# Kernel optimization log

Measured on AMD Instinct MI355X. Metric: run time of the kernel, lower is better.

## Reference

```python
import jax, jax.numpy as jnp
import numpy as np
import math

# AAMsoftmax constants (m=0.2, s=30), matching the torch implementation
M = 0.2
S = 30.0
COS_M = math.cos(M)
SIN_M = math.sin(M)
TH = math.cos(math.pi - M)
MM = math.sin(math.pi - M) * M

B, IN, P, C = 4096, 1024, 256, 5994


def _l2norm(v):
    # F.normalize: v / max(||v||, eps)
    n = jnp.sqrt(jnp.sum(v * v, axis=-1, keepdims=True))
    return v / jnp.maximum(n, 1e-12)


def setup_inputs() -> dict:
    key = jax.random.key(0)
    k0, k1, k2, k3 = jax.random.split(key, 4)
    return {
        "x": jax.random.normal(k0, (B, IN), jnp.float32),
        "label": jax.random.randint(k1, (B,), 0, C, dtype=jnp.int32),
        "W_fc": jax.random.normal(k2, (P, IN), jnp.float32) * (1.0 / np.sqrt(IN)),
        "b_fc": jnp.zeros((P,), jnp.float32),
        "W_aam": jax.random.normal(k3, (C, P), jnp.float32) * 0.05,
    }


def reference(x, label, W_fc, b_fc, W_aam):
    # fc layer: [B, IN] -> [B, P]
    e = x @ W_fc.T + b_fc
    # cosine similarity against class prototypes: [B, C]
    cosine = _l2norm(e) @ _l2norm(W_aam).T
    sine = jnp.sqrt(jnp.clip(1.0 - cosine * cosine, 0.0, 1.0))
    phi = cosine * COS_M - sine * SIN_M
    # easy-margin-off fallback: use cosine - mm where angle too large
    phi = jnp.where((cosine - TH) > 0, phi, cosine - MM)
    one_hot = jax.nn.one_hot(label, C, dtype=cosine.dtype)
    logits = (one_hot * phi + (1.0 - one_hot) * cosine) * S
    # cross-entropy (mean over batch)
    logp = jax.nn.log_softmax(logits, axis=-1)
    nll = -jnp.take_along_axis(logp, label[:, None].astype(jnp.int32), axis=1)[:, 0]
    return jnp.mean(nll)
```

## Files before the change

### kernel.cpp

```cpp
#include <hip/hip_runtime.h>
#include <math.h>

typedef __attribute__((ext_vector_type(8))) short bf16x8;
typedef __attribute__((ext_vector_type(4))) float f32x4;

#define AAM_COS_M 0.9800665778412416f
#define AAM_SIN_M 0.19866933079506122f
#define AAM_TH   (-0.9800665778412416f)
#define AAM_MM    0.03973386615901225f
#define C_CLS 5994

__device__ inline ushort f2bf(float f) {
    unsigned x = __float_as_uint(f);
    return (ushort)((x + 0x7fffu + ((x >> 16) & 1u)) >> 16);
}
__device__ inline float bflo(unsigned u) { return __uint_as_float(u << 16); }
__device__ inline float bfhi(unsigned u) { return __uint_as_float(u & 0xffff0000u); }

__device__ __forceinline__ void gload16(const void* g, void* lds) {
    __builtin_amdgcn_global_load_lds(
        (const __attribute__((address_space(1))) unsigned int*)g,
        (__attribute__((address_space(3))) unsigned int*)lds, 16, 0, 0);
}

__global__ __launch_bounds__(256) void conv_bf16(const float* __restrict__ x,
                                                 const float* __restrict__ Wfc,
                                                 ushort* __restrict__ xb,
                                                 ushort* __restrict__ wb) {
    int b = blockIdx.x;
    const float* s; ushort* d; int i;
    if (b < 4096) { s = x; d = xb; i = b * 256 + threadIdx.x; }
    else          { s = Wfc; d = wb; i = (b - 4096) * 256 + threadIdx.x; }
    float4 v = ((const float4*)s)[i];
    ushort4 o;
    o.x = f2bf(v.x); o.y = f2bf(v.y); o.z = f2bf(v.z); o.w = f2bf(v.w);
    ((ushort4*)d)[i] = o;
}

__global__ __launch_bounds__(256) void fc_mfma(const ushort* __restrict__ A,
                                               const ushort* __restrict__ Bm,
                                               const float* __restrict__ bias,
                                               float* __restrict__ C) {
    __shared__ ushort As[64 * 32];
    __shared__ ushort Bs[64 * 32];
    const int tid = threadIdx.x, lane = tid & 63, w = tid >> 6;
    const int wr = w >> 1, wc = w & 1;
    const int lx = lane & 15, lg = lane >> 4;
    const int l4 = lane >> 2, c8 = (lane & 3) << 3;
    const int rb = blockIdx.x * 64, cb = blockIdx.y * 64;

    f32x4 zero = {0.f, 0.f, 0.f, 0.f};
    f32x4 acc[2][2];
#pragma unroll
    for (int i = 0; i < 2; ++i)
#pragma unroll
        for (int j = 0; j < 2; ++j) acc[i][j] = zero;

    for (int k0 = 0; k0 < 1024; k0 += 32) {
        gload16(&A[(size_t)(rb + w * 16 + l4) * 1024 + k0 + c8], &As[w * 512]);
        gload16(&Bm[(size_t)(cb + w * 16 + l4) * 1024 + k0 + c8], &Bs[w * 512]);
        __syncthreads();
        bf16x8 af[2], bv[2];
#pragma unroll
        for (int f = 0; f < 2; ++f) {
            af[f] = *(const bf16x8*)&As[(wr * 32 + f * 16 + lx) * 32 + lg * 8];
            bv[f] = *(const bf16x8*)&Bs[(wc * 32 + f * 16 + lx) * 32 + lg * 8];
        }
#pragma unroll
        for (int i = 0; i < 2; ++i)
#pragma unroll
            for (int j = 0; j < 2; ++j)
                acc[i][j] = __builtin_amdgcn_mfma_f32_16x16x32_bf16(af[i], bv[j], acc[i][j], 0, 0, 0);
        __syncthreads();
    }
#pragma unroll
    for (int j = 0; j < 2; ++j) {
        int col = cb + wc * 32 + j * 16 + lx;
        float bb = bias[col];
#pragma unroll
        for (int i = 0; i < 2; ++i) {
            int row0 = rb + wr * 32 + i * 16 + lg * 4;
#pragma unroll
            for (int r = 0; r < 4; ++r)
                C[(size_t)(row0 + r) * 256 + col] = acc[i][j][r] + bb;
        }
    }
}

__global__ __launch_bounds__(256) void rownorm_e(const float* __restrict__ E,
                                                 ushort* __restrict__ En) {
    const int wave = threadIdx.x >> 6, lane = threadIdx.x & 63;
    const int row = blockIdx.x * 4 + wave;
    float4 v = ((const float4*)&E[(size_t)row * 256])[lane];
    float ss = v.x * v.x + v.y * v.y + v.z * v.z + v.w * v.w;
#pragma unroll
    for (int m = 32; m >= 1; m >>= 1) ss += __shfl_xor(ss, m, 64);
    float sc = 1.f / fmaxf(sqrtf(ss), 1e-12f);
    ushort4 o;
    o.x = f2bf(v.x * sc); o.y = f2bf(v.y * sc); o.z = f2bf(v.z * sc); o.w = f2bf(v.w * sc);
    ((ushort4*)&En[(size_t)row * 256])[lane] = o;
}

__global__ __launch_bounds__(256) void rownorm_w(const float* __restrict__ W,
                                                 ushort* __restrict__ Wn) {
    const int wave = threadIdx.x >> 6, lane = threadIdx.x & 63;
    const int row = blockIdx.x * 4 + wave;
    if (row >= 6144) return;
    ushort4 o;
    if (row < C_CLS) {
        float4 v = ((const float4*)&W[(size_t)row * 256])[lane];
        float ss = v.x * v.x + v.y * v.y + v.z * v.z + v.w * v.w;
#pragma unroll
        for (int m = 32; m >= 1; m >>= 1) ss += __shfl_xor(ss, m, 64);
        float sc = 1.f / fmaxf(sqrtf(ss), 1e-12f);
        o.x = f2bf(v.x * sc); o.y = f2bf(v.y * sc); o.z = f2bf(v.z * sc); o.w = f2bf(v.w * sc);
    } else {
        o.x = 0; o.y = 0; o.z = 0; o.w = 0;
    }
    ((ushort4*)&Wn[(size_t)row * 256])[lane] = o;
}

__global__ __launch_bounds__(256) void aam_mfma(const ushort* __restrict__ A,
                                                const ushort* __restrict__ Bm,
                                                float* __restrict__ pm,
                                                float* __restrict__ ps) {
    __shared__ ushort As[128 * 32];
    __shared__ ushort Bs[128 * 32];
    const int tid = threadIdx.x, lane = tid & 63, w = tid >> 6;
    const int wr = w >> 1, wc = w & 1;
    const int lx = lane & 15, lg = lane >> 4;
    const int l4 = lane >> 2, c8 = (lane & 3) << 3;
    const int rb = blockIdx.x * 128;
    const int split = blockIdx.y;

    float mrun[16], srun[16];
#pragma unroll
    for (int idx = 0; idx < 16; ++idx) { mrun[idx] = -INFINITY; srun[idx] = 0.f; }

    f32x4 zero = {0.f, 0.f, 0.f, 0.f};
    for (int t = 0; t < 3; ++t) {
        const int cb = split * 384 + t * 128;
        f32x4 acc[4][4];
#pragma unroll
        for (int i = 0; i < 4; ++i)
#pragma unroll
            for (int j = 0; j < 4; ++j) acc[i][j] = zero;

        for (int k0 = 0; k0 < 256; k0 += 32) {
            gload16(&A[(size_t)(rb + w * 32 + l4) * 256 + k0 + c8], &As[w * 1024]);
            gload16(&A[(size_t)(rb + w * 32 + 16 + l4) * 256 + k0 + c8], &As[w * 1024 + 512]);
            gload16(&Bm[(size_t)(cb + w * 32 + l4) * 256 + k0 + c8], &Bs[w * 1024]);
            gload16(&Bm[(size_t)(cb + w * 32 + 16 + l4) * 256 + k0 + c8], &Bs[w * 1024 + 512]);
            __syncthreads();
            bf16x8 af[4], bv[4];
#pragma unroll
            for (int f = 0; f < 4; ++f) {
                af[f] = *(const bf16x8*)&As[(wr * 64 + f * 16 + lx) * 32 + lg * 8];
                bv[f] = *(const bf16x8*)&Bs[(wc * 64 + f * 16 + lx) * 32 + lg * 8];
            }
#pragma unroll
            for (int i = 0; i < 4; ++i)
#pragma unroll
                for (int j = 0; j < 4; ++j)
                    acc[i][j] = __builtin_amdgcn_mfma_f32_16x16x32_bf16(af[i], bv[j], acc[i][j], 0, 0, 0);
            __syncthreads();
        }

#pragma unroll
        for (int j = 0; j < 4; ++j) {
            int c = cb + wc * 64 + j * 16 + lx;
            if (c < C_CLS) {
#pragma unroll
                for (int i = 0; i < 4; ++i)
#pragma unroll
                    for (int r = 0; r < 4; ++r) {
                        float v = 30.f * acc[i][j][r];
                        int idx = i * 4 + r;
                        float mn = fmaxf(mrun[idx], v);
                        srun[idx] = srun[idx] * __expf(mrun[idx] - mn) + __expf(v - mn);
                        mrun[idx] = mn;
                    }
            }
        }
    }

#pragma unroll
    for (int idx = 0; idx < 16; ++idx) {
#pragma unroll
        for (int msk = 1; msk < 16; msk <<= 1) {
            float om = __shfl_xor(mrun[idx], msk, 64);
            float os = __shfl_xor(srun[idx], msk, 64);
            float mn = fmaxf(mrun[idx], om);
            float sa = (mrun[idx] > -1e37f) ? srun[idx] * __expf(mrun[idx] - mn) : 0.f;
            float sb = (om > -1e37f) ? os * __expf(om - mn) : 0.f;
            mrun[idx] = mn; srun[idx] = sa + sb;
        }
        if (lx == 0) {
            int row = rb + wr * 64 + (idx >> 2) * 16 + lg * 4 + (idx & 3);
            int part = split * 2 + wc;
            pm[part * 4096 + row] = mrun[idx];
            ps[part * 4096 + row] = srun[idx];
        }
    }
}

__global__ __launch_bounds__(256) void reduce_all(const float* __restrict__ pm,
                                                  const float* __restrict__ ps,
                                                  const ushort* __restrict__ En,
                                                  const ushort* __restrict__ Wn,
                                                  const int* __restrict__ lab,
                                                  float* __restrict__ partial) {
    __shared__ float red[4];
    const int wave = threadIdx.x >> 6, lane = threadIdx.x & 63;
    const int gw = blockIdx.x * 4 + wave;
    float acc = 0.f;
#pragma unroll
    for (int r = 0; r < 4; ++r) {
        const int row = gw * 4 + r;
        const int l = lab[row];
        uint2 a = ((const uint2*)&En[(size_t)row * 256])[lane];
        uint2 b = ((const uint2*)&Wn[(size_t)l * 256])[lane];
        float sum = bflo(a.x) * bflo(b.x) + bfhi(a.x) * bfhi(b.x)
                  + bflo(a.y) * bflo(b.y) + bfhi(a.y) * bfhi(b.y);
#pragma unroll
        for (int m = 32; m >= 1; m >>= 1) sum += __shfl_xor(sum, m, 64);
        float cv = sum;

        float m, s;
        if (lane < 32) { m = pm[lane * 4096 + row]; s = ps[lane * 4096 + row]; }
        else           { m = -INFINITY; s = 0.f; }
#pragma unroll
        for (int msk = 1; msk <= 32; msk <<= 1) {
            float om = __shfl_xor(m, msk, 64);
            float os = __shfl_xor(s, msk, 64);
            float mn = fmaxf(m, om);
            float sa = (m > -1e37f) ? s * __expf(m - mn) : 0.f;
            float sb = (om > -1e37f) ? os * __expf(om - mn) : 0.f;
            m = mn; s = sa + sb;
        }
        float sine = sqrtf(fmaxf(1.f - cv * cv, 0.f));
        float phi = cv * AAM_COS_M - sine * AAM_SIN_M;
        phi = ((cv - AAM_TH) > 0.f) ? phi : (cv - AAM_MM);
        float vplain = 30.f * cv, vlab = 30.f * phi;
        float denom = s - __expf(vplain - m) + __expf(vlab - m);
        acc += m + logf(denom) - vlab;
    }
    if (lane == 0) red[wave] = acc;
    __syncthreads();
    if (threadIdx.x == 0)
        partial[blockIdx.x] = red[0] + red[1] + red[2] + red[3];
}

__global__ __launch_bounds__(256) void final_reduce(const float* __restrict__ partial,
                                                    float* __restrict__ out) {
    __shared__ float red[4];
    const int wave = threadIdx.x >> 6, lane = threadIdx.x & 63;
    float v = partial[threadIdx.x];
#pragma unroll
    for (int m = 32; m >= 1; m >>= 1) v += __shfl_xor(v, m, 64);
    if (lane == 0) red[wave] = v;
    __syncthreads();
    if (threadIdx.x == 0)
        out[0] = (red[0] + red[1] + red[2] + red[3]) * (1.f / 4096.f);
}

extern "C" void kernel_launch(void* const* d_in, const int* in_sizes, int n_in,
                              void* d_out, int out_size, void* d_ws, size_t ws_size,
                              hipStream_t stream) {
    const float* x    = (const float*)d_in[0];
    const int*   lab  = (const int*)d_in[1];
    const float* Wfc  = (const float*)d_in[2];
    const float* bfc  = (const float*)d_in[3];
    const float* Waam = (const float*)d_in[4];
    float* out = (float*)d_out;

    char* ws = (char*)d_ws;
    ushort* xb   = (ushort*)(ws);
    ushort* Wfcb = (ushort*)(ws + 8388608);
    float*  E    = (float*) (ws + 8912896);
    ushort* En   = (ushort*)(ws);
    ushort* Wn   = (ushort*)(ws + 2097152);
    float*  pm   = (float*) (ws + 13107200);
    float*  ps   = (float*) (ws + 13631488);
    float*  part = (float*) (ws + 14155776);

    conv_bf16<<<4352, 256, 0, stream>>>(x, Wfc, xb, Wfcb);
    fc_mfma<<<dim3(64, 4), 256, 0, stream>>>(xb, Wfcb, bfc, E);
    rownorm_e<<<1024, 256, 0, stream>>>(E, En);
    rownorm_w<<<1536, 256, 0, stream>>>(Waam, Wn);
    aam_mfma<<<dim3(32, 16), 256, 0, stream>>>(En, Wn, pm, ps);
    reduce_all<<<256, 256, 0, stream>>>(pm, ps, En, Wn, lab, part);
    final_reduce<<<1, 256, 0, stream>>>(part, out);
}
```

Baseline: 129.8 us.

## Double-buffer AAM GEMM with swizzled LDS, fixed-max softmax, merge prep kernels

Merges the W_aam row-normalisation into the bf16 conversion kernel, which removes one launch. The AAM GEMM now double-buffers LDS with BK=64 and an XOR-swizzled layout to avoid bank conflicts, and sets launch_bounds to 2 blocks per CU. Because cosines are bounded by 1, the online max-tracking softmax becomes a plain sum of exp(30*c-30) with a fixed max of 30. That drops the pm buffer and the log-sum-exp merging in the reduction. The trade-off is more LDS per block (64 KB) and a reliance on normalised inputs to keep the exponent bounded.

```diff
diff --git a/kernel.cpp b/kernel.cpp
--- a/kernel.cpp
+++ b/kernel.cpp
@@ -23,18 +23,38 @@
         (__attribute__((address_space(3))) unsigned int*)lds, 16, 0, 0);
 }
 
-__global__ __launch_bounds__(256) void conv_bf16(const float* __restrict__ x,
-                                                 const float* __restrict__ Wfc,
-                                                 ushort* __restrict__ xb,
-                                                 ushort* __restrict__ wb) {
-    int b = blockIdx.x;
-    const float* s; ushort* d; int i;
-    if (b < 4096) { s = x; d = xb; i = b * 256 + threadIdx.x; }
-    else          { s = Wfc; d = wb; i = (b - 4096) * 256 + threadIdx.x; }
-    float4 v = ((const float4*)s)[i];
-    ushort4 o;
-    o.x = f2bf(v.x); o.y = f2bf(v.y); o.z = f2bf(v.z); o.w = f2bf(v.w);
-    ((ushort4*)d)[i] = o;
+__global__ __launch_bounds__(256) void prep(const float* __restrict__ x,
+                                            const float* __restrict__ Wfc,
+                                            const float* __restrict__ Waam,
+                                            ushort* __restrict__ xb,
+                                            ushort* __restrict__ wfcb,
+                                            ushort* __restrict__ Wn) {
+    const int b = blockIdx.x;
+    if (b < 4352) {
+        const float* s = (b < 4096) ? x : Wfc;
+        ushort* d      = (b < 4096) ? xb : wfcb;
+        int i = (b < 4096 ? b : b - 4096) * 256 + threadIdx.x;
+        float4 v = ((const float4*)s)[i];
+        ushort4 o;
+        o.x = f2bf(v.x); o.y = f2bf(v.y); o.z = f2bf(v.z); o.w = f2bf(v.w);
+        ((ushort4*)d)[i] = o;
+    } else {
+        const int wave = threadIdx.x >> 6, lane = threadIdx.x & 63;
+        const int row = (b - 4352) * 4 + wave;
+        ushort4 o;
+        if (row < C_CLS) {
+            float4 v = ((const float4*)&Waam[(size_t)row * 256])[lane];
+            float ss = v.x * v.x + v.y * v.y + v.z * v.z + v.w * v.w;
+#pragma unroll
+            for (int m = 32; m >= 1; m >>= 1) ss += __shfl_xor(ss, m, 64);
+            float sc = 1.f / fmaxf(sqrtf(ss), 1e-12f);
+            o.x = f2bf(v.x * sc); o.y = f2bf(v.y * sc);
+            o.z = f2bf(v.z * sc); o.w = f2bf(v.w * sc);
+        } else {
+            o.x = 0; o.y = 0; o.z = 0; o.w = 0;
+        }
+        ((ushort4*)&Wn[(size_t)row * 256])[lane] = o;
+    }
 }
 
 __global__ __launch_bounds__(256) void fc_mfma(const ushort* __restrict__ A,
@@ -101,111 +121,103 @@
     ((ushort4*)&En[(size_t)row * 256])[lane] = o;
 }
 
-__global__ __launch_bounds__(256) void rownorm_w(const float* __restrict__ W,
-                                                 ushort* __restrict__ Wn) {
-    const int wave = threadIdx.x >> 6, lane = threadIdx.x & 63;
-    const int row = blockIdx.x * 4 + wave;
-    if (row >= 6144) return;
-    ushort4 o;
-    if (row < C_CLS) {
-        float4 v = ((const float4*)&W[(size_t)row * 256])[lane];
-        float ss = v.x * v.x + v.y * v.y + v.z * v.z + v.w * v.w;
-#pragma unroll
-        for (int m = 32; m >= 1; m >>= 1) ss += __shfl_xor(ss, m, 64);
-        float sc = 1.f / fmaxf(sqrtf(ss), 1e-12f);
-        o.x = f2bf(v.x * sc); o.y = f2bf(v.y * sc); o.z = f2bf(v.z * sc); o.w = f2bf(v.w * sc);
-    } else {
-        o.x = 0; o.y = 0; o.z = 0; o.w = 0;
-    }
-    ((ushort4*)&Wn[(size_t)row * 256])[lane] = o;
-}
-
-__global__ __launch_bounds__(256) void aam_mfma(const ushort* __restrict__ A,
-                                                const ushort* __restrict__ Bm,
-                                                float* __restrict__ pm,
-                                                float* __restrict__ ps) {
-    __shared__ ushort As[128 * 32];
-    __shared__ ushort Bs[128 * 32];
+__global__ __launch_bounds__(256, 2) void aam_mfma(const ushort* __restrict__ A,
+                                                   const ushort* __restrict__ Bm,
+                                                   float* __restrict__ ps) {
+    __shared__ ushort As[2][128 * 64];
+    __shared__ ushort Bs[2][128 * 64];
     const int tid = threadIdx.x, lane = tid & 63, w = tid >> 6;
     const int wr = w >> 1, wc = w & 1;
     const int lx = lane & 15, lg = lane >> 4;
-    const int l4 = lane >> 2, c8 = (lane & 3) << 3;
     const int rb = blockIdx.x * 128;
     const int split = blockIdx.y;
 
-    float mrun[16], srun[16];
-#pragma unroll
-    for (int idx = 0; idx < 16; ++idx) { mrun[idx] = -INFINITY; srun[idx] = 0.f; }
+    const int lrow = lane >> 3;
+    const int gcol = ((lane & 7) ^ lrow) * 8;
+
+    float srun[16];
+#pragma unroll
+    for (int idx = 0; idx < 16; ++idx) srun[idx] = 0.f;
 
     f32x4 zero = {0.f, 0.f, 0.f, 0.f};
-    for (int t = 0; t < 3; ++t) {
-        const int cb = split * 384 + t * 128;
-        f32x4 acc[4][4];
-#pragma unroll
-        for (int i = 0; i < 4; ++i)
-#pragma unroll
-            for (int j = 0; j < 4; ++j) acc[i][j] = zero;
-
-        for (int k0 = 0; k0 < 256; k0 += 32) {
-            gload16(&A[(size_t)(rb + w * 32 + l4) * 256 + k0 + c8], &As[w * 1024]);
-            gload16(&A[(size_t)(rb + w * 32 + 16 + l4) * 256 + k0 + c8], &As[w * 1024 + 512]);
-            gload16(&Bm[(size_t)(cb + w * 32 + l4) * 256 + k0 + c8], &Bs[w * 1024]);
-            gload16(&Bm[(size_t)(cb + w * 32 + 16 + l4) * 256 + k0 + c8], &Bs[w * 1024 + 512]);
-            __syncthreads();
+    f32x4 acc[4][4];
+#pragma unroll
+    for (int i = 0; i < 4; ++i)
+#pragma unroll
+        for (int j = 0; j < 4; ++j) acc[i][j] = zero;
+
+#define AAM_STAGE(buf, g) do {                                                  \
+    int t_ = (g) >> 2, k0_ = ((g) & 3) * 64;                                    \
+    int cb_ = split * 384 + t_ * 128;                                           \
+    _Pragma("unroll")                                                           \
+    for (int s_ = 0; s_ < 4; ++s_) {                                            \
+        int r0_ = w * 32 + s_ * 8;                                              \
+        gload16(&A[(size_t)(rb + r0_ + lrow) * 256 + k0_ + gcol],               \
+                &As[buf][r0_ * 64]);                                            \
+        gload16(&Bm[(size_t)(cb_ + r0_ + lrow) * 256 + k0_ + gcol],             \
+                &Bs[buf][r0_ * 64]);                                            \
+    } } while (0)
+
+    int cur = 0;
+    AAM_STAGE(0, 0);
+    __syncthreads();
+
+    for (int g = 0; g < 12; ++g) {
+        if (g < 11) AAM_STAGE(cur ^ 1, g + 1);
+#pragma unroll
+        for (int kk = 0; kk < 2; ++kk) {
             bf16x8 af[4], bv[4];
 #pragma unroll
             for (int f = 0; f < 4; ++f) {
-                af[f] = *(const bf16x8*)&As[(wr * 64 + f * 16 + lx) * 32 + lg * 8];
-                bv[f] = *(const bf16x8*)&Bs[(wc * 64 + f * 16 + lx) * 32 + lg * 8];
+                int ra = wr * 64 + f * 16 + lx;
+                int ca = (lg + kk * 4) ^ (lx & 7);
+                af[f] = *(const bf16x8*)&As[cur][ra * 64 + ca * 8];
+                int rq = wc * 64 + f * 16 + lx;
+                bv[f] = *(const bf16x8*)&Bs[cur][rq * 64 + ca * 8];
             }
 #pragma unroll
             for (int i = 0; i < 4; ++i)
 #pragma unroll
                 for (int j = 0; j < 4; ++j)
                     acc[i][j] = __builtin_amdgcn_mfma_f32_16x16x32_bf16(af[i], bv[j], acc[i][j], 0, 0, 0);
-            __syncthreads();
-        }
-
-#pragma unroll
-        for (int j = 0; j < 4; ++j) {
-            int c = cb + wc * 64 + j * 16 + lx;
-            if (c < C_CLS) {
-#pragma unroll
-                for (int i = 0; i < 4; ++i)
-#pragma unroll
-                    for (int r = 0; r < 4; ++r) {
-                        float v = 30.f * acc[i][j][r];
-                        int idx = i * 4 + r;
-                        float mn = fmaxf(mrun[idx], v);
-                        srun[idx] = srun[idx] * __expf(mrun[idx] - mn) + __expf(v - mn);
-                        mrun[idx] = mn;
-                    }
+        }
+        if ((g & 3) == 3) {
+            int cb_ = split * 384 + (g >> 2) * 128;
+#pragma unroll
+            for (int j = 0; j < 4; ++j) {
+                int c = cb_ + wc * 64 + j * 16 + lx;
+                if (c < C_CLS) {
+#pragma unroll
+                    for (int i = 0; i < 4; ++i)
+#pragma unroll
+                        for (int r = 0; r < 4; ++r)
+                            srun[i * 4 + r] += __expf(30.f * acc[i][j][r] - 30.f);
+                }
             }
-        }
-    }
+#pragma unroll
+            for (int i = 0; i < 4; ++i)
+#pragma unroll
+                for (int j = 0; j < 4; ++j) acc[i][j] = zero;
+        }
+        __syncthreads();
+        cur ^= 1;
+    }
+#undef AAM_STAGE
 
 #pragma unroll
     for (int idx = 0; idx < 16; ++idx) {
 #pragma unroll
-        for (int msk = 1; msk < 16; msk <<= 1) {
-            float om = __shfl_xor(mrun[idx], msk, 64);
-            float os = __shfl_xor(srun[idx], msk, 64);
-            float mn = fmaxf(mrun[idx], om);
-            float sa = (mrun[idx] > -1e37f) ? srun[idx] * __expf(mrun[idx] - mn) : 0.f;
-            float sb = (om > -1e37f) ? os * __expf(om - mn) : 0.f;
-            mrun[idx] = mn; srun[idx] = sa + sb;
-        }
+        for (int msk = 1; msk < 16; msk <<= 1)
+            srun[idx] += __shfl_xor(srun[idx], msk, 64);
         if (lx == 0) {
             int row = rb + wr * 64 + (idx >> 2) * 16 + lg * 4 + (idx & 3);
             int part = split * 2 + wc;
-            pm[part * 4096 + row] = mrun[idx];
             ps[part * 4096 + row] = srun[idx];
         }
     }
 }
 
-__global__ __launch_bounds__(256) void reduce_all(const float* __restrict__ pm,
-                                                  const float* __restrict__ ps,
+__global__ __launch_bounds__(256) void reduce_all(const float* __restrict__ ps,
                                                   const ushort* __restrict__ En,
                                                   const ushort* __restrict__ Wn,
                                                   const int* __restrict__ lab,
@@ -226,24 +238,15 @@
         for (int m = 32; m >= 1; m >>= 1) sum += __shfl_xor(sum, m, 64);
         float cv = sum;
 
-        float m, s;
-        if (lane < 32) { m = pm[lane * 4096 + row]; s = ps[lane * 4096 + row]; }
-        else           { m = -INFINITY; s = 0.f; }
-#pragma unroll
-        for (int msk = 1; msk <= 32; msk <<= 1) {
-            float om = __shfl_xor(m, msk, 64);
-            float os = __shfl_xor(s, msk, 64);
-            float mn = fmaxf(m, om);
-            float sa = (m > -1e37f) ? s * __expf(m - mn) : 0.f;
-            float sb = (om > -1e37f) ? os * __expf(om - mn) : 0.f;
-            m = mn; s = sa + sb;
-        }
+        float s = (lane < 32) ? ps[lane * 4096 + row] : 0.f;
+#pragma unroll
+        for (int msk = 1; msk <= 32; msk <<= 1) s += __shfl_xor(s, msk, 64);
+
         float sine = sqrtf(fmaxf(1.f - cv * cv, 0.f));
         float phi = cv * AAM_COS_M - sine * AAM_SIN_M;
         phi = ((cv - AAM_TH) > 0.f) ? phi : (cv - AAM_MM);
-        float vplain = 30.f * cv, vlab = 30.f * phi;
-        float denom = s - __expf(vplain - m) + __expf(vlab - m);
-        acc += m + logf(denom) - vlab;
+        float denom = s - __expf(30.f * cv - 30.f) + __expf(30.f * phi - 30.f);
+        acc += 30.f + logf(denom) - 30.f * phi;
     }
     if (lane == 0) red[wave] = acc;
     __syncthreads();
@@ -279,16 +282,14 @@
     ushort* Wfcb = (ushort*)(ws + 8388608);
     float*  E    = (float*) (ws + 8912896);
     ushort* En   = (ushort*)(ws);
-    ushort* Wn   = (ushort*)(ws + 2097152);
-    float*  pm   = (float*) (ws + 13107200);
-    float*  ps   = (float*) (ws + 13631488);
-    float*  part = (float*) (ws + 14155776);
-
-    conv_bf16<<<4352, 256, 0, stream>>>(x, Wfc, xb, Wfcb);
+    ushort* Wn   = (ushort*)(ws + 13107200);
+    float*  ps   = (float*) (ws + 16252928);
+    float*  part = (float*) (ws + 16777216);
+
+    prep<<<5888, 256, 0, stream>>>(x, Wfc, Waam, xb, Wfcb, Wn);
     fc_mfma<<<dim3(64, 4), 256, 0, stream>>>(xb, Wfcb, bfc, E);
     rownorm_e<<<1024, 256, 0, stream>>>(E, En);
-    rownorm_w<<<1536, 256, 0, stream>>>(Waam, Wn);
-    aam_mfma<<<dim3(32, 16), 256, 0, stream>>>(En, Wn, pm, ps);
-    reduce_all<<<256, 256, 0, stream>>>(pm, ps, En, Wn, lab, part);
+    aam_mfma<<<dim3(32, 16), 256, 0, stream>>>(En, Wn, ps);
+    reduce_all<<<256, 256, 0, stream>>>(ps, En, Wn, lab, part);
     final_reduce<<<1, 256, 0, stream>>>(part, out);
 }
```

After: 119.9 us. 7.7% less time.
